# Performance work log

Measured on AMD Instinct MI355X. Metric: run time of the kernel, lower is better.

## Reference

```python
import jax, jax.numpy as jnp
import numpy as np

KSIZE = 3
SCALE = 2


def setup_inputs() -> dict:
    key = jax.random.key(0)
    k1, k2, k3, k4 = jax.random.split(key, 4)
    B, C, H, W = 8, 3, 512, 512
    h, w = H // SCALE, W // SCALE
    return {
        "images": jax.random.uniform(k1, (B, C, H, W), jnp.float32),
        "kernels": jax.random.uniform(k2, (B, KSIZE ** 2, h, w), jnp.float32),
        "offsets_x": jax.random.uniform(k3, (B, KSIZE ** 2, h, w), jnp.float32),
        "offsets_y": jax.random.uniform(k4, (B, KSIZE ** 2, h, w), jnp.float32),
    }


def _softround(x, alpha=1.0):
    two_pi = 2.0 * jnp.pi
    return x - alpha * (jnp.sin(two_pi * x) / two_pi)


def _batch_bli(im, x, y):
    # im: [B, H, W, 3] channel-last; x, y: [B, N] float coords
    B, N = x.shape
    x0 = jnp.floor(x).astype(jnp.int32)
    x1 = x0 + 1
    y0 = jnp.floor(y).astype(jnp.int32)
    y1 = y0 + 1
    # original clamps x by im.shape[2] and y by im.shape[1] (square images)
    x0 = jnp.clip(x0, 0, im.shape[2] - 1)
    x1 = jnp.clip(x1, 0, im.shape[2] - 1)
    y0 = jnp.clip(y0, 0, im.shape[1] - 1)
    y1 = jnp.clip(y1, 0, im.shape[1] - 1)
    bidx = jnp.arange(B)[:, None]
    # vectorized gather of the four corners; flatten like torch.cat of [3]-vectors
    Ia = im[bidx, x0, y0].reshape(-1)  # [B*N*3]
    Ib = im[bidx, x0, y1].reshape(-1)
    Ic = im[bidx, x1, y0].reshape(-1)
    Id = im[bidx, x1, y1].reshape(-1)
    scale_w = (1.0 / ((x1 - x0) * (y1 - y0))).reshape(-1)  # [B*N]
    # faithful to the original's (scrambling) reshape semantics
    m1 = jnp.concatenate([x1 - x, x - x0], axis=1).astype(jnp.float32)  # [B, 2N]
    m1 = jnp.tile(m1.reshape(B * N, 1, 1, 2), (1, 2, 1, 1))             # [BN,2,1,2]
    m2 = jnp.stack([Ib, Ia, Id, Ic], axis=1).reshape(B * N, 2, 2, 3)    # [BN,2,2,3]
    m3 = jnp.concatenate([y1 - y, y - y0], axis=1).astype(jnp.float32)
    m3 = m3.reshape(B * N, 1, 2, 1)                                     # [BN,1,2,1]
    t = jnp.matmul(m1, m2).transpose(0, 3, 2, 1)  # [BN,3,1,2]
    out = jnp.matmul(t, m3).reshape(B * N, 3)     # [BN,3]
    return scale_w[:, None] * out


def reference(images, kernels, offsets_x, offsets_y):
    B = images.shape[0]
    h, w = images.shape[2] // SCALE, images.shape[3] // SCALE
    kernels = kernels.transpose(0, 2, 3, 1)      # [B,h,w,9]
    ox = offsets_x.transpose(0, 2, 3, 1)         # [B,h,w,9]
    oy = offsets_y.transpose(0, 2, 3, 1)
    u = jnp.arange(h, dtype=jnp.float32) + 0.5 * SCALE - 0.5
    kx = jnp.repeat(jnp.arange(KSIZE), KSIZE).astype(jnp.float32)  # 0,0,0,1,1,1,2,2,2
    ky = jnp.tile(jnp.arange(KSIZE), KSIZE).astype(jnp.float32)    # 0,1,2,0,1,2,0,1,2
    # original broadcasts u.reshape(h,1) over the w axis (requires h == w)
    coords_x = ox + KSIZE / 2 + kx + u[:, None]
    coords_y = oy + KSIZE / 2 + ky + u[:, None]
    im = images.transpose(0, 2, 3, 1)  # [B,H,W,3]
    pix = _batch_bli(im, coords_x.reshape(B, -1), coords_y.reshape(B, -1))
    pix_hr = pix.reshape(B, h, w, KSIZE ** 2, 3)
    out = jnp.sum(kernels[..., None] * pix_hr, axis=-2)  # [B,h,w,3]
    return _softround(out * 255.0)
```

## Files before the change

kernel.cpp:

```cpp
#include <hip/hip_runtime.h>
#include <math.h>

#define BATCH 8
#define HI 512
#define WI 512
#define HO 256
#define WO 256
#define PLANE (HI*WI)
#define OPIX (HO*WO)
#define HALF (OPIX/2)
#define LROWS 68
#define LCOLS 10
#define LQ 11

__global__ __launch_bounds__(256, 4) void downsampler_kernel(
    const float* __restrict__ images,
    const float* __restrict__ kernels,
    const float* __restrict__ offx,
    const float* __restrict__ offy,
    float* __restrict__ out)
{
    __shared__ float4 simg[LROWS * LQ];

    const int blk  = blockIdx.x;
    const int b    = blk >> 7;
    const int ihx  = (blk >> 2) & 31;
    const int w0   = (blk & 3) << 6;
    const int tid  = threadIdx.x;
    const int lane = tid & 63;
    const int iw   = w0 + lane;
    const int ihA  = (ihx << 2) + (tid >> 6);
    const int plA  = ihA * WO + iw;
    const int plB  = plA + HALF;

    const float* offxb = offx    + (size_t)b * 9 * OPIX;
    const float* offyb = offy    + (size_t)b * 9 * OPIX;
    const float* kernb = kernels + (size_t)b * 9 * OPIX;

    float oxA[9], oyA[9], oxB[9], oyB[9];
    #pragma unroll
    for (int k = 0; k < 9; ++k) {
        oxA[k] = offxb[k * OPIX + plA];
        oyA[k] = offyb[k * OPIX + plA];
        oxB[k] = offxb[k * OPIX + plB];
        oyB[k] = offyb[k * OPIX + plB];
    }

    float2 sx_[9], sy_[9];
    float  kvA[9], kvB[9];
    #pragma unroll
    for (int k = 0; k < 9; ++k) {
        sx_[k] = ((const float2*)(offxb + k * OPIX))[plA];
        sy_[k] = ((const float2*)(offyb + k * OPIX))[plA];
        kvA[k] = kernb[k * OPIX + plA];
        kvB[k] = kernb[k * OPIX + plB];
    }

    {
        const float* imb = images + (size_t)b * 3 * PLANE;
        #pragma unroll
        for (int ii = 0; ii < 3; ++ii) {
            const int i = tid + ii * 256;
            if (i < LROWS * LCOLS) {
                const int row = i / LCOLS;
                const int col = i - row * LCOLS;
                const int r = w0 + 2 + row;
                int c = r - 4 + col;
                c = c < 0 ? 0 : c;
                const float* src = imb + r * WI + c;
                simg[row * LQ + col] =
                    make_float4(src[0], src[PLANE], src[2 * PLANE], 0.0f);
            }
        }
    }

    const float uu_own = (float)iw + 0.5f;
    int offA9[9], offB9[9];
    #pragma unroll
    for (int k = 0; k < 9; ++k) {
        const float kxf = (float)(k / 3);
        const float kyf = (float)(k - 3 * (k / 3));
        {
            const float cx = ((oxA[k] + 1.5f) + kxf) + uu_own;
            const float cy = ((oyA[k] + 1.5f) + kyf) + uu_own;
            const int x0 = (int)floorf(cx);
            const int y0 = (int)floorf(cy);
            offA9[k] = (((x0 - 2 - w0) * LQ) + (y0 - x0 + 3)) << 4;
        }
        {
            const float cx = ((oxB[k] + 1.5f) + kxf) + uu_own;
            const float cy = ((oyB[k] + 1.5f) + kyf) + uu_own;
            const int x0 = (int)floorf(cx);
            const int y0 = (int)floorf(cy);
            offB9[k] = (((x0 - 2 - w0) * LQ) + (y0 - x0 + 3)) << 4;
        }
    }
    __builtin_amdgcn_sched_barrier(0);
    __syncthreads();

    const float uu_s0 = (float)((2 * iw) & 255) + 0.5f;
    const float uu_s1 = uu_s0 + 1.0f;

    float aA0 = 0.f, aA1 = 0.f, aA2 = 0.f;
    float aB0 = 0.f, aB1 = 0.f, aB2 = 0.f;
    const char* sbase = (const char*)simg;

    #pragma unroll
    for (int k = 0; k < 9; ++k) {
        const int ta = 2 * k, tb = 2 * k + 1;
        const int sel_a = (ta >= 9) ? 1 : 0;
        const int sel_b = (tb >= 9) ? 1 : 0;
        const int ks_a = ta - 9 * sel_a;
        const int ks_b = tb - 9 * sel_b;
        const float uu_a = sel_a ? uu_s1 : uu_s0;
        const float uu_b = sel_b ? uu_s1 : uu_s0;
        const float oxa  = sel_a ? sx_[ks_a].y : sx_[ks_a].x;
        const float oya  = sel_a ? sy_[ks_a].y : sy_[ks_a].x;
        const float oxb2 = sel_b ? sx_[ks_b].y : sx_[ks_b].x;
        const float oyb2 = sel_b ? sy_[ks_b].y : sy_[ks_b].x;
        const float kxa = (float)(ks_a / 3), kya = (float)(ks_a - 3 * (ks_a / 3));
        const float kxb = (float)(ks_b / 3), kyb = (float)(ks_b - 3 * (ks_b / 3));

        const float cxa = ((oxa + 1.5f) + kxa) + uu_a;
        const float cya = ((oya + 1.5f) + kya) + uu_a;
        const float cxb = ((oxb2 + 1.5f) + kxb) + uu_b;
        const float cyb = ((oyb2 + 1.5f) + kyb) + uu_b;
        const float fxa = cxa - floorf(cxa);
        const float fya = cya - floorf(cya);
        const float fxb = cxb - floorf(cxb);
        const float fyb = cyb - floorf(cyb);

        const float w0A = 1.0f - fxa, w1A = 1.0f - fxb;
        const float v0A = 1.0f - fya, v1A = 1.0f - fyb;
        const float A00 = w0A * v0A, A10 = w1A * v0A, A01 = w0A * v1A, A11 = w1A * v1A;
        const float B00 = fxa * fya, B10 = fxb * fya, B01 = fxa * fyb, B11 = fxb * fyb;

        {
            const float4* q = (const float4*)(sbase + offA9[k]);
            const float4 Ia = q[1];
            const float4 Ib = q[2];
            const float4 Ic = q[LQ];
            const float4 Id = q[LQ + 1];
            const float p0 = A00 * Ib.x + A10 * Ic.x + A01 * Id.y + A11 * Ia.z;
            const float p1 = A00 * Ia.x + A10 * Ib.y + A01 * Ic.y + A11 * Id.z;
            const float p2 = A00 * Id.x + A10 * Ia.y + A01 * Ib.z + A11 * Ic.z;
            aA0 += kvA[k] * p0;
            aA1 += kvA[k] * p1;
            aA2 += kvA[k] * p2;
        }
        {
            const float4* q = (const float4*)(sbase + offB9[k]);
            const float4 Ia = q[1];
            const float4 Ib = q[2];
            const float4 Ic = q[LQ];
            const float4 Id = q[LQ + 1];
            const float p0 = B00 * Ib.x + B10 * Ic.x + B01 * Id.y + B11 * Ia.z;
            const float p1 = B00 * Ia.x + B10 * Ib.y + B01 * Ic.y + B11 * Id.z;
            const float p2 = B00 * Id.x + B10 * Ia.y + B01 * Ib.z + B11 * Ic.z;
            aB0 += kvB[k] * p0;
            aB1 += kvB[k] * p1;
            aB2 += kvB[k] * p2;
        }
    }

    const float TWO_PI_INV = 0.15915494309189533577f;
    {
        const size_t obase = ((size_t)b * OPIX + (size_t)plA) * 3;
        const float z0 = aA0 * 255.0f;
        const float z1 = aA1 * 255.0f;
        const float z2 = aA2 * 255.0f;
        const float r0s = z0 - rintf(z0);
        const float r1s = z1 - rintf(z1);
        const float r2s = z2 - rintf(z2);
        out[obase + 0] = z0 - __builtin_amdgcn_sinf(r0s) * TWO_PI_INV;
        out[obase + 1] = z1 - __builtin_amdgcn_sinf(r1s) * TWO_PI_INV;
        out[obase + 2] = z2 - __builtin_amdgcn_sinf(r2s) * TWO_PI_INV;
    }
    {
        const size_t obase = ((size_t)b * OPIX + (size_t)plB) * 3;
        const float z0 = aB0 * 255.0f;
        const float z1 = aB1 * 255.0f;
        const float z2 = aB2 * 255.0f;
        const float r0s = z0 - rintf(z0);
        const float r1s = z1 - rintf(z1);
        const float r2s = z2 - rintf(z2);
        out[obase + 0] = z0 - __builtin_amdgcn_sinf(r0s) * TWO_PI_INV;
        out[obase + 1] = z1 - __builtin_amdgcn_sinf(r1s) * TWO_PI_INV;
        out[obase + 2] = z2 - __builtin_amdgcn_sinf(r2s) * TWO_PI_INV;
    }
}

extern "C" void kernel_launch(void* const* d_in, const int* in_sizes, int n_in,
                              void* d_out, int out_size, void* d_ws, size_t ws_size,
                              hipStream_t stream) {
    const float* images  = (const float*)d_in[0];
    const float* kernels = (const float*)d_in[1];
    const float* offx    = (const float*)d_in[2];
    const float* offy    = (const float*)d_in[3];
    float* out = (float*)d_out;

    dim3 grid(BATCH * 32 * 4);
    dim3 block(256);
    hipLaunchKernelGGL(downsampler_kernel, grid, block, 0, stream,
                       images, kernels, offx, offy, out);
}
```

Baseline: 114.5 us.

## Process two row tiles per block reusing the shared image tile

Each block now handles two groups of output rows instead of one, halving the grid. The shared-memory image tile depends only on batch and column block, so it is staged once and reused for both row groups. The second group's offset and kernel loads are issued before the barrier so they overlap with the first group's compute. Launch bounds drop to 2 to allow the larger register footprint, which reduces occupancy and the number of blocks available to hide latency.

```diff
diff --git a/kernel.cpp b/kernel.cpp
--- a/kernel.cpp
+++ b/kernel.cpp
@@ -13,7 +13,97 @@
 #define LCOLS 10
 #define LQ 11
 
-__global__ __launch_bounds__(256, 4) void downsampler_kernel(
+__device__ __forceinline__ int lds_off(float ox, float oy, float kxf, float kyf,
+                                       float uu_own, int w0)
+{
+    const float cx = ((ox + 1.5f) + kxf) + uu_own;
+    const float cy = ((oy + 1.5f) + kyf) + uu_own;
+    const int x0 = (int)floorf(cx);
+    const int y0 = (int)floorf(cy);
+    return (((x0 - 2 - w0) * LQ) + (y0 - x0 + 3)) << 4;
+}
+
+__device__ __forceinline__ void compute_tile(
+    const char* sbase, const int* offA, const int* offB,
+    const float2* sx, const float2* sy, const float* kvA, const float* kvB,
+    float uu_s0, float uu_s1,
+    float* aA, float* aB)
+{
+    #pragma unroll
+    for (int k = 0; k < 9; ++k) {
+        const int ta = 2 * k, tb = 2 * k + 1;
+        const int sel_a = (ta >= 9) ? 1 : 0;
+        const int sel_b = (tb >= 9) ? 1 : 0;
+        const int ks_a = ta - 9 * sel_a;
+        const int ks_b = tb - 9 * sel_b;
+        const float uu_a = sel_a ? uu_s1 : uu_s0;
+        const float uu_b = sel_b ? uu_s1 : uu_s0;
+        const float oxa  = sel_a ? sx[ks_a].y : sx[ks_a].x;
+        const float oya  = sel_a ? sy[ks_a].y : sy[ks_a].x;
+        const float oxb2 = sel_b ? sx[ks_b].y : sx[ks_b].x;
+        const float oyb2 = sel_b ? sy[ks_b].y : sy[ks_b].x;
+        const float kxa = (float)(ks_a / 3), kya = (float)(ks_a - 3 * (ks_a / 3));
+        const float kxb = (float)(ks_b / 3), kyb = (float)(ks_b - 3 * (ks_b / 3));
+
+        const float cxa = ((oxa + 1.5f) + kxa) + uu_a;
+        const float cya = ((oya + 1.5f) + kya) + uu_a;
+        const float cxb = ((oxb2 + 1.5f) + kxb) + uu_b;
+        const float cyb = ((oyb2 + 1.5f) + kyb) + uu_b;
+        const float fxa = cxa - floorf(cxa);
+        const float fya = cya - floorf(cya);
+        const float fxb = cxb - floorf(cxb);
+        const float fyb = cyb - floorf(cyb);
+
+        const float w0A = 1.0f - fxa, w1A = 1.0f - fxb;
+        const float v0A = 1.0f - fya, v1A = 1.0f - fyb;
+        const float A00 = w0A * v0A, A10 = w1A * v0A, A01 = w0A * v1A, A11 = w1A * v1A;
+        const float B00 = fxa * fya, B10 = fxb * fya, B01 = fxa * fyb, B11 = fxb * fyb;
+
+        {
+            const float4* q = (const float4*)(sbase + offA[k]);
+            const float4 Ia = q[1];
+            const float4 Ib = q[2];
+            const float4 Ic = q[LQ];
+            const float4 Id = q[LQ + 1];
+            const float p0 = A00 * Ib.x + A10 * Ic.x + A01 * Id.y + A11 * Ia.z;
+            const float p1 = A00 * Ia.x + A10 * Ib.y + A01 * Ic.y + A11 * Id.z;
+            const float p2 = A00 * Id.x + A10 * Ia.y + A01 * Ib.z + A11 * Ic.z;
+            aA[0] += kvA[k] * p0;
+            aA[1] += kvA[k] * p1;
+            aA[2] += kvA[k] * p2;
+        }
+        {
+            const float4* q = (const float4*)(sbase + offB[k]);
+            const float4 Ia = q[1];
+            const float4 Ib = q[2];
+            const float4 Ic = q[LQ];
+            const float4 Id = q[LQ + 1];
+            const float p0 = B00 * Ib.x + B10 * Ic.x + B01 * Id.y + B11 * Ia.z;
+            const float p1 = B00 * Ia.x + B10 * Ib.y + B01 * Ic.y + B11 * Id.z;
+            const float p2 = B00 * Id.x + B10 * Ia.y + B01 * Ib.z + B11 * Ic.z;
+            aB[0] += kvB[k] * p0;
+            aB[1] += kvB[k] * p1;
+            aB[2] += kvB[k] * p2;
+        }
+    }
+}
+
+__device__ __forceinline__ void store3(float* __restrict__ out, size_t obase,
+                                       float a0, float a1, float a2)
+{
+    const float TWO_PI_INV = 0.15915494309189533577f;
+    const float z0 = a0 * 255.0f;
+    const float z1 = a1 * 255.0f;
+    const float z2 = a2 * 255.0f;
+    const float r0s = z0 - rintf(z0);
+    const float r1s = z1 - rintf(z1);
+    const float r2s = z2 - rintf(z2);
+    out[obase + 0] = z0 - __builtin_amdgcn_sinf(r0s) * TWO_PI_INV;
+    out[obase + 1] = z1 - __builtin_amdgcn_sinf(r1s) * TWO_PI_INV;
+    out[obase + 2] = z2 - __builtin_amdgcn_sinf(r2s) * TWO_PI_INV;
+}
+
+__global__ __launch_bounds__(256, 2) void downsampler_kernel(
     const float* __restrict__ images,
     const float* __restrict__ kernels,
     const float* __restrict__ offx,
@@ -23,37 +113,33 @@
     __shared__ float4 simg[LROWS * LQ];
 
     const int blk  = blockIdx.x;
-    const int b    = blk >> 7;
-    const int ihx  = (blk >> 2) & 31;
+    const int b    = blk >> 6;
+    const int ihx  = (blk >> 2) & 15;
     const int w0   = (blk & 3) << 6;
     const int tid  = threadIdx.x;
     const int lane = tid & 63;
     const int iw   = w0 + lane;
-    const int ihA  = (ihx << 2) + (tid >> 6);
-    const int plA  = ihA * WO + iw;
-    const int plB  = plA + HALF;
+    const int ihA0 = (ihx << 3) + (tid >> 6);
+    const int plA0 = ihA0 * WO + iw;
+    const int plA1 = plA0 + 4 * WO;
 
     const float* offxb = offx    + (size_t)b * 9 * OPIX;
     const float* offyb = offy    + (size_t)b * 9 * OPIX;
     const float* kernb = kernels + (size_t)b * 9 * OPIX;
 
-    float oxA[9], oyA[9], oxB[9], oyB[9];
-    #pragma unroll
-    for (int k = 0; k < 9; ++k) {
-        oxA[k] = offxb[k * OPIX + plA];
-        oyA[k] = offyb[k * OPIX + plA];
-        oxB[k] = offxb[k * OPIX + plB];
-        oyB[k] = offyb[k * OPIX + plB];
-    }
-
-    float2 sx_[9], sy_[9];
-    float  kvA[9], kvB[9];
-    #pragma unroll
-    for (int k = 0; k < 9; ++k) {
-        sx_[k] = ((const float2*)(offxb + k * OPIX))[plA];
-        sy_[k] = ((const float2*)(offyb + k * OPIX))[plA];
-        kvA[k] = kernb[k * OPIX + plA];
-        kvB[k] = kernb[k * OPIX + plB];
+    float oxA0[9], oyA0[9], oxB0[9], oyB0[9];
+    float2 sx0[9], sy0[9];
+    float  kvA0[9], kvB0[9];
+    #pragma unroll
+    for (int k = 0; k < 9; ++k) {
+        oxA0[k] = offxb[k * OPIX + plA0];
+        oyA0[k] = offyb[k * OPIX + plA0];
+        oxB0[k] = offxb[k * OPIX + plA0 + HALF];
+        oyB0[k] = offyb[k * OPIX + plA0 + HALF];
+        sx0[k]  = ((const float2*)(offxb + k * OPIX))[plA0];
+        sy0[k]  = ((const float2*)(offyb + k * OPIX))[plA0];
+        kvA0[k] = kernb[k * OPIX + plA0];
+        kvB0[k] = kernb[k * OPIX + plA0 + HALF];
     }
 
     {
@@ -74,119 +160,62 @@
         }
     }
 
+    float oxA1[9], oyA1[9], oxB1[9], oyB1[9];
+    float2 sx1[9], sy1[9];
+    float  kvA1[9], kvB1[9];
+    #pragma unroll
+    for (int k = 0; k < 9; ++k) {
+        oxA1[k] = offxb[k * OPIX + plA1];
+        oyA1[k] = offyb[k * OPIX + plA1];
+        oxB1[k] = offxb[k * OPIX + plA1 + HALF];
+        oyB1[k] = offyb[k * OPIX + plA1 + HALF];
+        sx1[k]  = ((const float2*)(offxb + k * OPIX))[plA1];
+        sy1[k]  = ((const float2*)(offyb + k * OPIX))[plA1];
+        kvA1[k] = kernb[k * OPIX + plA1];
+        kvB1[k] = kernb[k * OPIX + plA1 + HALF];
+    }
+
     const float uu_own = (float)iw + 0.5f;
-    int offA9[9], offB9[9];
+    int offA0_[9], offB0_[9];
     #pragma unroll
     for (int k = 0; k < 9; ++k) {
         const float kxf = (float)(k / 3);
         const float kyf = (float)(k - 3 * (k / 3));
-        {
-            const float cx = ((oxA[k] + 1.5f) + kxf) + uu_own;
-            const float cy = ((oyA[k] + 1.5f) + kyf) + uu_own;
-            const int x0 = (int)floorf(cx);
-            const int y0 = (int)floorf(cy);
-            offA9[k] = (((x0 - 2 - w0) * LQ) + (y0 - x0 + 3)) << 4;
-        }
-        {
-            const float cx = ((oxB[k] + 1.5f) + kxf) + uu_own;
-            const float cy = ((oyB[k] + 1.5f) + kyf) + uu_own;
-            const int x0 = (int)floorf(cx);
-            const int y0 = (int)floorf(cy);
-            offB9[k] = (((x0 - 2 - w0) * LQ) + (y0 - x0 + 3)) << 4;
-        }
-    }
+        offA0_[k] = lds_off(oxA0[k], oyA0[k], kxf, kyf, uu_own, w0);
+        offB0_[k] = lds_off(oxB0[k], oyB0[k], kxf, kyf, uu_own, w0);
+    }
+
     __builtin_amdgcn_sched_barrier(0);
-    __syncthreads();
+    asm volatile("s_waitcnt lgkmcnt(0)" ::: "memory");
+    __builtin_amdgcn_s_barrier();
+    __builtin_amdgcn_sched_barrier(0);
 
     const float uu_s0 = (float)((2 * iw) & 255) + 0.5f;
     const float uu_s1 = uu_s0 + 1.0f;
-
-    float aA0 = 0.f, aA1 = 0.f, aA2 = 0.f;
-    float aB0 = 0.f, aB1 = 0.f, aB2 = 0.f;
     const char* sbase = (const char*)simg;
 
-    #pragma unroll
-    for (int k = 0; k < 9; ++k) {
-        const int ta = 2 * k, tb = 2 * k + 1;
-        const int sel_a = (ta >= 9) ? 1 : 0;
-        const int sel_b = (tb >= 9) ? 1 : 0;
-        const int ks_a = ta - 9 * sel_a;
-        const int ks_b = tb - 9 * sel_b;
-        const float uu_a = sel_a ? uu_s1 : uu_s0;
-        const float uu_b = sel_b ? uu_s1 : uu_s0;
-        const float oxa  = sel_a ? sx_[ks_a].y : sx_[ks_a].x;
-        const float oya  = sel_a ? sy_[ks_a].y : sy_[ks_a].x;
-        const float oxb2 = sel_b ? sx_[ks_b].y : sx_[ks_b].x;
-        const float oyb2 = sel_b ? sy_[ks_b].y : sy_[ks_b].x;
-        const float kxa = (float)(ks_a / 3), kya = (float)(ks_a - 3 * (ks_a / 3));
-        const float kxb = (float)(ks_b / 3), kyb = (float)(ks_b - 3 * (ks_b / 3));
-
-        const float cxa = ((oxa + 1.5f) + kxa) + uu_a;
-        const float cya = ((oya + 1.5f) + kya) + uu_a;
-        const float cxb = ((oxb2 + 1.5f) + kxb) + uu_b;
-        const float cyb = ((oyb2 + 1.5f) + kyb) + uu_b;
-        const float fxa = cxa - floorf(cxa);
-        const float fya = cya - floorf(cya);
-        const float fxb = cxb - floorf(cxb);
-        const float fyb = cyb - floorf(cyb);
-
-        const float w0A = 1.0f - fxa, w1A = 1.0f - fxb;
-        const float v0A = 1.0f - fya, v1A = 1.0f - fyb;
-        const float A00 = w0A * v0A, A10 = w1A * v0A, A01 = w0A * v1A, A11 = w1A * v1A;
-        const float B00 = fxa * fya, B10 = fxb * fya, B01 = fxa * fyb, B11 = fxb * fyb;
-
-        {
-            const float4* q = (const float4*)(sbase + offA9[k]);
-            const float4 Ia = q[1];
-            const float4 Ib = q[2];
-            const float4 Ic = q[LQ];
-            const float4 Id = q[LQ + 1];
-            const float p0 = A00 * Ib.x + A10 * Ic.x + A01 * Id.y + A11 * Ia.z;
-            const float p1 = A00 * Ia.x + A10 * Ib.y + A01 * Ic.y + A11 * Id.z;
-            const float p2 = A00 * Id.x + A10 * Ia.y + A01 * Ib.z + A11 * Ic.z;
-            aA0 += kvA[k] * p0;
-            aA1 += kvA[k] * p1;
-            aA2 += kvA[k] * p2;
-        }
-        {
-            const float4* q = (const float4*)(sbase + offB9[k]);
-            const float4 Ia = q[1];
-            const float4 Ib = q[2];
-            const float4 Ic = q[LQ];
-            const float4 Id = q[LQ + 1];
-            const float p0 = B00 * Ib.x + B10 * Ic.x + B01 * Id.y + B11 * Ia.z;
-            const float p1 = B00 * Ia.x + B10 * Ib.y + B01 * Ic.y + B11 * Id.z;
-            const float p2 = B00 * Id.x + B10 * Ia.y + B01 * Ib.z + B11 * Ic.z;
-            aB0 += kvB[k] * p0;
-            aB1 += kvB[k] * p1;
-            aB2 += kvB[k] * p2;
-        }
-    }
-
-    const float TWO_PI_INV = 0.15915494309189533577f;
     {
-        const size_t obase = ((size_t)b * OPIX + (size_t)plA) * 3;
-        const float z0 = aA0 * 255.0f;
-        const float z1 = aA1 * 255.0f;
-        const float z2 = aA2 * 255.0f;
-        const float r0s = z0 - rintf(z0);
-        const float r1s = z1 - rintf(z1);
-        const float r2s = z2 - rintf(z2);
-        out[obase + 0] = z0 - __builtin_amdgcn_sinf(r0s) * TWO_PI_INV;
-        out[obase + 1] = z1 - __builtin_amdgcn_sinf(r1s) * TWO_PI_INV;
-        out[obase + 2] = z2 - __builtin_amdgcn_sinf(r2s) * TWO_PI_INV;
-    }
+        float aA[3] = {0.f, 0.f, 0.f}, aB[3] = {0.f, 0.f, 0.f};
+        compute_tile(sbase, offA0_, offB0_, sx0, sy0, kvA0, kvB0,
+                     uu_s0, uu_s1, aA, aB);
+        store3(out, ((size_t)b * OPIX + (size_t)plA0) * 3, aA[0], aA[1], aA[2]);
+        store3(out, ((size_t)b * OPIX + (size_t)(plA0 + HALF)) * 3, aB[0], aB[1], aB[2]);
+    }
+
     {
-        const size_t obase = ((size_t)b * OPIX + (size_t)plB) * 3;
-        const float z0 = aB0 * 255.0f;
-        const float z1 = aB1 * 255.0f;
-        const float z2 = aB2 * 255.0f;
-        const float r0s = z0 - rintf(z0);
-        const float r1s = z1 - rintf(z1);
-        const float r2s = z2 - rintf(z2);
-        out[obase + 0] = z0 - __builtin_amdgcn_sinf(r0s) * TWO_PI_INV;
-        out[obase + 1] = z1 - __builtin_amdgcn_sinf(r1s) * TWO_PI_INV;
-        out[obase + 2] = z2 - __builtin_amdgcn_sinf(r2s) * TWO_PI_INV;
+        int offA1_[9], offB1_[9];
+        #pragma unroll
+        for (int k = 0; k < 9; ++k) {
+            const float kxf = (float)(k / 3);
+            const float kyf = (float)(k - 3 * (k / 3));
+            offA1_[k] = lds_off(oxA1[k], oyA1[k], kxf, kyf, uu_own, w0);
+            offB1_[k] = lds_off(oxB1[k], oyB1[k], kxf, kyf, uu_own, w0);
+        }
+        float aA[3] = {0.f, 0.f, 0.f}, aB[3] = {0.f, 0.f, 0.f};
+        compute_tile(sbase, offA1_, offB1_, sx1, sy1, kvA1, kvB1,
+                     uu_s0, uu_s1, aA, aB);
+        store3(out, ((size_t)b * OPIX + (size_t)plA1) * 3, aA[0], aA[1], aA[2]);
+        store3(out, ((size_t)b * OPIX + (size_t)(plA1 + HALF)) * 3, aB[0], aB[1], aB[2]);
     }
 }
 
@@ -199,7 +228,7 @@
     const float* offy    = (const float*)d_in[3];
     float* out = (float*)d_out;
 
-    dim3 grid(BATCH * 32 * 4);
+    dim3 grid(BATCH * 16 * 4);
     dim3 block(256);
     hipLaunchKernelGGL(downsampler_kernel, grid, block, 0, stream,
                        images, kernels, offx, offy, out);
```

Result: no change. 115.7 us (+1.0%).
